# Kernel tuning notes

Measured on AMD Instinct MI355X. Metric: run time of the kernel, lower is better.

The kernel has to match this reference:

```python
import jax, jax.numpy as jnp
import numpy as np

N_NODES = 100000
N_EDGES = 3200000


def gcn_conv(x, src, dst, W, b, n):
    # x: [N, Fin] -> linear transform then symmetric-normalized scatter-add (PyG GCNConv)
    xw = x @ W  # [N, Fout]
    loop = jnp.arange(n, dtype=src.dtype)
    s = jnp.concatenate([src, loop])  # add self-loops
    d = jnp.concatenate([dst, loop])
    deg = jax.ops.segment_sum(jnp.ones_like(s, dtype=xw.dtype), d, num_segments=n)
    dinv = jnp.where(deg > 0, jax.lax.rsqrt(deg), 0.0)
    norm = dinv[s] * dinv[d]  # [E+N]
    out = jax.ops.segment_sum(xw[s] * norm[:, None], d, num_segments=n)
    return out + b


def setup_inputs() -> dict:
    key = jax.random.key(0)
    ks = jax.random.split(key, 11)
    x = jax.random.normal(ks[0], (N_NODES, 2), dtype=jnp.float32)
    edge_index = jax.random.randint(ks[1], (2, N_EDGES), 0, N_NODES, dtype=jnp.int64)
    W1 = jax.random.normal(ks[2], (2, 32), dtype=jnp.float32) * 0.5
    b1 = jax.random.normal(ks[3], (32,), dtype=jnp.float32) * 0.1
    W2 = jax.random.normal(ks[4], (32, 32), dtype=jnp.float32) * 0.18
    b2 = jax.random.normal(ks[5], (32,), dtype=jnp.float32) * 0.1
    Wf1 = jax.random.normal(ks[6], (32, 32), dtype=jnp.float32) * 0.18
    bf1 = jax.random.normal(ks[7], (32,), dtype=jnp.float32) * 0.1
    Wf2 = jax.random.normal(ks[8], (32, 1), dtype=jnp.float32) * 0.18
    bf2 = jax.random.normal(ks[9], (1,), dtype=jnp.float32) * 0.1
    return {"x": x, "edge_index": edge_index, "W1": W1, "b1": b1, "W2": W2,
            "b2": b2, "Wf1": Wf1, "bf1": bf1, "Wf2": Wf2, "bf2": bf2}


def reference(x, edge_index, W1, b1, W2, b2, Wf1, bf1, Wf2, bf2):
    n = x.shape[0]
    src, dst = edge_index[0], edge_index[1]
    h = jax.nn.relu(gcn_conv(x, src, dst, W1, b1, n))
    h = jax.nn.relu(gcn_conv(h, src, dst, W2, b2, n))
    h = jax.nn.relu(h @ Wf1 + bf1)
    return h @ Wf2 + bf2  # [N, 1]
```

## Files before the change

### kernel.cpp

```cpp
#include <hip/hip_runtime.h>

#define NGRP 512
#define CAP  6656
#define EPB  8192
#define NE   16
#define SRC_BITS 17
#define SRC_MASK 0x1FFFF

static __device__ __forceinline__ unsigned short f2bf(float f) {
    unsigned u = __float_as_uint(f);
    return (unsigned short)((u + 0x7FFFu + ((u >> 16) & 1u)) >> 16);
}
static __device__ __forceinline__ float bf2f_lo(unsigned u) { return __uint_as_float(u << 16); }
static __device__ __forceinline__ float bf2f_hi(unsigned u) { return __uint_as_float(u & 0xFFFF0000u); }


__global__ void k_init(int* gcursor) {
    gcursor[threadIdx.x] = threadIdx.x * CAP;
}

__global__ __launch_bounds__(512) void k_partition(const int* __restrict__ ei, int* gcursor,
                                                   unsigned* __restrict__ pairs,
                                                   int E, int n, int GN) {
    __shared__ int cnt[NGRP];
    __shared__ int cur[NGRP];
    int tid = threadIdx.x;
    cnt[tid] = 0;
    __syncthreads();
    int base = blockIdx.x * EPB;
    int sreg[NE], dreg[NE];
#pragma unroll
    for (int k = 0; k < NE; ++k) {
        int e = base + tid + k * 512;
        int d = -1, s = 0;
        if (e < E) {
            s = ei[e];
            d = ei[E + e];
            if ((unsigned)s < (unsigned)n && (unsigned)d < (unsigned)n)
                atomicAdd(&cnt[d / GN], 1);
            else d = -1;
        }
        sreg[k] = s; dreg[k] = d;
    }
    __syncthreads();
    { int c = cnt[tid]; cur[tid] = c ? atomicAdd(&gcursor[tid], c) : 0; }
    __syncthreads();
#pragma unroll
    for (int k = 0; k < NE; ++k) {
        int d = dreg[k];
        if (d >= 0) {
            int g = d / GN;
            int w = atomicAdd(&cur[g], 1);
            if (w < (g + 1) * CAP)
                pairs[w] = ((unsigned)(d - g * GN) << SRC_BITS) | (unsigned)sreg[k];
        }
    }
}

__global__ __launch_bounds__(512) void k_build(const int* __restrict__ gcursor,
                                               const unsigned* __restrict__ pairs,
                                               const float2* __restrict__ x2,
                                               int* __restrict__ rowStart, int* __restrict__ rowEnd,
                                               int* __restrict__ srclist, float* __restrict__ dinv,
                                               float2* __restrict__ z, int n, int GN) {
    __shared__ unsigned pl[CAP];
    __shared__ int cnt[512];
    __shared__ int cur[512];
    int g = blockIdx.x;
    int t = threadIdx.x;
    int gbeg = g * CAP;
    int gend = gcursor[g];
    int cape = gbeg + CAP;
    if (gend > cape) gend = cape;
    int m = gend - gbeg;
    cnt[t] = 0;
    __syncthreads();
    for (int k = t; k < m; k += 512) {
        unsigned v = pairs[gbeg + k];
        pl[k] = v;
        atomicAdd(&cnt[(v >> SRC_BITS) & 511], 1);
    }
    __syncthreads();
    int c = cnt[t];
    for (int off = 1; off < 512; off <<= 1) {
        int add = (t >= off) ? cnt[t - off] : 0;
        __syncthreads();
        cnt[t] += add;
        __syncthreads();
    }
    int excl = cnt[t] - c;
    int node = g * GN + t;
    if (t < GN && node < n) {
        int st = gbeg + excl;
        rowStart[node] = st;
        rowEnd[node] = st + c;
        float di = rsqrtf(1.0f + (float)c);
        dinv[node] = di;
        float2 xv = x2[node];
        z[node] = make_float2(xv.x * di, xv.y * di);
    }
    cur[t] = excl;
    __syncthreads();
    for (int k = t; k < m; k += 512) {
        unsigned v = pl[k];
        int dl = (v >> SRC_BITS) & 511;
        int pos = atomicAdd(&cur[dl], 1);
        srclist[gbeg + pos] = (int)(v & SRC_MASK);
    }
}


__global__ __launch_bounds__(256) void k_gather2f(const int* __restrict__ rowStart,
                                                  const int* __restrict__ rowEnd,
                                                  const int* __restrict__ srclist,
                                                  const float2* __restrict__ z,
                                                  float2* __restrict__ agg, int n) {
    int w = blockIdx.x * 256 + threadIdx.x;
    if (w >= n) return;
    int e = rowStart[w], end = rowEnd[w];
    float ax = 0.f, ay = 0.f;
    for (; e + 4 <= end; e += 4) {
        int s0 = srclist[e], s1 = srclist[e + 1], s2 = srclist[e + 2], s3 = srclist[e + 3];
        float2 v0 = z[s0], v1 = z[s1], v2 = z[s2], v3 = z[s3];
        ax += v0.x + v1.x + v2.x + v3.x;
        ay += v0.y + v1.y + v2.y + v3.y;
    }
    for (; e < end; ++e) {
        float2 v = z[srclist[e]];
        ax += v.x; ay += v.y;
    }
    float2 v = z[w];
    agg[w] = make_float2(ax + v.x, ay + v.y);
}

__global__ void k_mid1(const float2* __restrict__ agg, const float* __restrict__ dinv,
                       const float* __restrict__ W1, const float* __restrict__ b1,
                       const float* __restrict__ W2, unsigned short* __restrict__ y0,
                       unsigned short* __restrict__ y1, int n) {
    __shared__ float sW[1024];
    __shared__ float sh[8][33];
    int tid = threadIdx.x;
    for (int k = tid; k < 1024; k += 256) sW[k] = W2[k];
    int ln = tid >> 5, f = tid & 31;
    int i = blockIdx.x * 8 + ln;
    float h = 0.f, di = 0.f;
    if (i < n) {
        di = dinv[i];
        float2 a = agg[i];
        h = di * (a.x * W1[f] + a.y * W1[32 + f]) + b1[f];
        h = h > 0.f ? h : 0.f;
    }
    sh[ln][f] = h;
    __syncthreads();
    if (i < n) {
        float acc = 0.f;
#pragma unroll
        for (int k = 0; k < 32; ++k) acc += sh[ln][k] * sW[k * 32 + f];
        unsigned short* yp = (f < 16) ? y0 : y1;
        yp[(size_t)i * 16 + (f & 15)] = f2bf(acc * di);
    }
}

#define ACC8(v)                                        \
    a0 += bf2f_lo((v).x); a1 += bf2f_hi((v).x);        \
    a2 += bf2f_lo((v).y); a3 += bf2f_hi((v).y);        \
    a4 += bf2f_lo((v).z); a5 += bf2f_hi((v).z);        \
    a6 += bf2f_lo((v).w); a7 += bf2f_hi((v).w);

__global__ __launch_bounds__(256) void k_gather_plane(const int* __restrict__ rowStart,
                                                      const int* __restrict__ rowEnd,
                                                      const int* __restrict__ srclist,
                                                      const uint4* __restrict__ yh,
                                                      float4* __restrict__ acc4, int n, int p) {
    int w = blockIdx.x * 64 + (threadIdx.x >> 2);
    if (w >= n) return;
    int slot = (threadIdx.x >> 1) & 1;
    int q = threadIdx.x & 1;
    int beg = rowStart[w], end = rowEnd[w];
    int deg = end - beg;
    int half = (deg + 1) >> 1;
    int e = beg + slot * half;
    int e1 = slot ? end : (beg + half);
    float a0 = 0.f, a1 = 0.f, a2 = 0.f, a3 = 0.f, a4 = 0.f, a5 = 0.f, a6 = 0.f, a7 = 0.f;
    for (; e + 4 <= e1; e += 4) {
        int s0 = srclist[e], s1 = srclist[e + 1], s2 = srclist[e + 2], s3 = srclist[e + 3];
        uint4 v0 = yh[(size_t)s0 * 2 + q];
        uint4 v1 = yh[(size_t)s1 * 2 + q];
        uint4 v2 = yh[(size_t)s2 * 2 + q];
        uint4 v3 = yh[(size_t)s3 * 2 + q];
        ACC8(v0); ACC8(v1); ACC8(v2); ACC8(v3);
    }
    for (; e < e1; ++e) {
        uint4 v = yh[(size_t)srclist[e] * 2 + q];
        ACC8(v);
    }
    if (slot == 0) {
        uint4 v = yh[(size_t)w * 2 + q];
        ACC8(v);
    }
    a0 += __shfl_xor(a0, 2, 64);
    a1 += __shfl_xor(a1, 2, 64);
    a2 += __shfl_xor(a2, 2, 64);
    a3 += __shfl_xor(a3, 2, 64);
    a4 += __shfl_xor(a4, 2, 64);
    a5 += __shfl_xor(a5, 2, 64);
    a6 += __shfl_xor(a6, 2, 64);
    a7 += __shfl_xor(a7, 2, 64);
    if (slot == 0) {
        float4* dst = acc4 + (size_t)w * 8 + p * 4 + q * 2;
        dst[0] = make_float4(a0, a1, a2, a3);
        dst[1] = make_float4(a4, a5, a6, a7);
    }
}

__global__ void k_final(const float* __restrict__ acc, const float* __restrict__ dinv,
                        const float* __restrict__ b2, const float* __restrict__ Wf1,
                        const float* __restrict__ bf1, const float* __restrict__ Wf2,
                        const float* __restrict__ bf2, float* __restrict__ out, int n) {
    __shared__ float sW[1024];
    __shared__ float sh[8][33];
    int tid = threadIdx.x;
    for (int k = tid; k < 1024; k += 256) sW[k] = Wf1[k];
    int ln = tid >> 5, f = tid & 31;
    int i = blockIdx.x * 8 + ln;
    float h = 0.f;
    if (i < n) {
        h = dinv[i] * acc[(size_t)i * 32 + f] + b2[f];
        h = h > 0.f ? h : 0.f;
    }
    sh[ln][f] = h;
    __syncthreads();
    float p = 0.f;
    if (i < n) {
        float a = bf1[f];
#pragma unroll
        for (int k = 0; k < 32; ++k) a += sh[ln][k] * sW[k * 32 + f];
        a = a > 0.f ? a : 0.f;
        p = a * Wf2[f];
    }
#pragma unroll
    for (int m = 16; m >= 1; m >>= 1) p += __shfl_xor(p, m, 64);
    if (f == 0 && i < n) out[i] = p + bf2[0];
}


extern "C" void kernel_launch(void* const* d_in, const int* in_sizes, int n_in,
                              void* d_out, int out_size, void* d_ws, size_t ws_size,
                              hipStream_t stream) {
    const float* x   = (const float*)d_in[0];
    const int*   ei  = (const int*)d_in[1];
    const float* W1  = (const float*)d_in[2];
    const float* b1  = (const float*)d_in[3];
    const float* W2  = (const float*)d_in[4];
    const float* b2  = (const float*)d_in[5];
    const float* Wf1 = (const float*)d_in[6];
    const float* bf1 = (const float*)d_in[7];
    const float* Wf2 = (const float*)d_in[8];
    const float* bf2 = (const float*)d_in[9];
    float* out = (float*)d_out;

    int n = in_sizes[0] / 2;
    int E = in_sizes[1] / 2;
    int GN = (n + NGRP - 1) / NGRP;

    float* wsf = (float*)d_ws;
    int*    srclist  = (int*)wsf;
    size_t  o = (size_t)NGRP * CAP;
    int*    rowStart = (int*)(wsf + o);     o += n;
    int*    rowEnd   = (int*)(wsf + o);     o += n;
    float*  dinv     = wsf + o;             o += n;
    float2* z        = (float2*)(wsf + o);  o += 2 * (size_t)n;
    float2* agg      = (float2*)(wsf + o);  o += 2 * (size_t)n;
    int*    gcursor  = (int*)(wsf + o);     o += NGRP;
    o = (o + 3) & ~(size_t)3;
    float*  acc      = wsf + o;             o += 32 * (size_t)n;
    unsigned short* y0 = (unsigned short*)(wsf + o);
    unsigned short* y1 = y0 + (size_t)n * 16;
    unsigned* pairs = (unsigned*)acc;

    const int B = 256;
    int nblk = (E + EPB - 1) / EPB;

    k_init<<<1, NGRP, 0, stream>>>(gcursor);
    k_partition<<<nblk, 512, 0, stream>>>(ei, gcursor, pairs, E, n, GN);
    k_build<<<NGRP, 512, 0, stream>>>(gcursor, pairs, (const float2*)x, rowStart, rowEnd,
                                      srclist, dinv, z, n, GN);

    k_gather2f<<<(n + 255) / 256, B, 0, stream>>>(rowStart, rowEnd, srclist, z, agg, n);
    k_mid1<<<(n + 7) / 8, B, 0, stream>>>(agg, dinv, W1, b1, W2, y0, y1, n);

    k_gather_plane<<<(n + 63) / 64, B, 0, stream>>>(rowStart, rowEnd, srclist,
                                                    (const uint4*)y0, (float4*)acc, n, 0);
    k_gather_plane<<<(n + 63) / 64, B, 0, stream>>>(rowStart, rowEnd, srclist,
                                                    (const uint4*)y1, (float4*)acc, n, 1);

    k_final<<<(n + 7) / 8, B, 0, stream>>>(acc, dinv, b2, Wf1, bf1, Wf2, bf2, out, n);
}
```

Before: 174.5 us.

## Fuse layer-1 gather into mid kernel and merge both plane gathers into one launch

```diff
diff --git a/kernel.cpp b/kernel.cpp
--- a/kernel.cpp
+++ b/kernel.cpp
@@ -110,44 +110,41 @@
 }
 
 
-__global__ __launch_bounds__(256) void k_gather2f(const int* __restrict__ rowStart,
-                                                  const int* __restrict__ rowEnd,
-                                                  const int* __restrict__ srclist,
-                                                  const float2* __restrict__ z,
-                                                  float2* __restrict__ agg, int n) {
-    int w = blockIdx.x * 256 + threadIdx.x;
-    if (w >= n) return;
-    int e = rowStart[w], end = rowEnd[w];
-    float ax = 0.f, ay = 0.f;
-    for (; e + 4 <= end; e += 4) {
-        int s0 = srclist[e], s1 = srclist[e + 1], s2 = srclist[e + 2], s3 = srclist[e + 3];
-        float2 v0 = z[s0], v1 = z[s1], v2 = z[s2], v3 = z[s3];
-        ax += v0.x + v1.x + v2.x + v3.x;
-        ay += v0.y + v1.y + v2.y + v3.y;
-    }
-    for (; e < end; ++e) {
-        float2 v = z[srclist[e]];
-        ax += v.x; ay += v.y;
-    }
-    float2 v = z[w];
-    agg[w] = make_float2(ax + v.x, ay + v.y);
-}
-
-__global__ void k_mid1(const float2* __restrict__ agg, const float* __restrict__ dinv,
-                       const float* __restrict__ W1, const float* __restrict__ b1,
-                       const float* __restrict__ W2, unsigned short* __restrict__ y0,
-                       unsigned short* __restrict__ y1, int n) {
+__global__ __launch_bounds__(256) void k_mid1f(const int* __restrict__ rowStart,
+                                               const int* __restrict__ rowEnd,
+                                               const int* __restrict__ srclist,
+                                               const float2* __restrict__ z,
+                                               const float* __restrict__ dinv,
+                                               const float* __restrict__ W1,
+                                               const float* __restrict__ b1,
+                                               const float* __restrict__ W2,
+                                               unsigned short* __restrict__ y0,
+                                               unsigned short* __restrict__ y1, int n) {
     __shared__ float sW[1024];
     __shared__ float sh[8][33];
     int tid = threadIdx.x;
     for (int k = tid; k < 1024; k += 256) sW[k] = W2[k];
     int ln = tid >> 5, f = tid & 31;
     int i = blockIdx.x * 8 + ln;
+    float ax = 0.f, ay = 0.f;
+    if (i < n) {
+        int e = rowStart[i] + f, end = rowEnd[i];
+        for (; e < end; e += 32) {
+            float2 v = z[srclist[e]];
+            ax += v.x; ay += v.y;
+        }
+    }
+#pragma unroll
+    for (int m = 1; m < 32; m <<= 1) {
+        ax += __shfl_xor(ax, m, 64);
+        ay += __shfl_xor(ay, m, 64);
+    }
     float h = 0.f, di = 0.f;
     if (i < n) {
         di = dinv[i];
-        float2 a = agg[i];
-        h = di * (a.x * W1[f] + a.y * W1[32 + f]) + b1[f];
+        float2 zz = z[i];
+        ax += zz.x; ay += zz.y;
+        h = di * (ax * W1[f] + ay * W1[32 + f]) + b1[f];
         h = h > 0.f ? h : 0.f;
     }
     sh[ln][f] = h;
@@ -156,8 +153,8 @@
         float acc = 0.f;
 #pragma unroll
         for (int k = 0; k < 32; ++k) acc += sh[ln][k] * sW[k * 32 + f];
-        unsigned short* yp = (f < 16) ? y0 : y1;
-        yp[(size_t)i * 16 + (f & 15)] = f2bf(acc * di);
+        unsigned short* ypl = (f < 16) ? y0 : y1;
+        ypl[(size_t)i * 16 + (f & 15)] = f2bf(acc * di);
     }
 }
 
@@ -167,12 +164,16 @@
     a4 += bf2f_lo((v).z); a5 += bf2f_hi((v).z);        \
     a6 += bf2f_lo((v).w); a7 += bf2f_hi((v).w);
 
-__global__ __launch_bounds__(256) void k_gather_plane(const int* __restrict__ rowStart,
-                                                      const int* __restrict__ rowEnd,
-                                                      const int* __restrict__ srclist,
-                                                      const uint4* __restrict__ yh,
-                                                      float4* __restrict__ acc4, int n, int p) {
-    int w = blockIdx.x * 64 + (threadIdx.x >> 2);
+__global__ __launch_bounds__(256) void k_gather_planes(const int* __restrict__ rowStart,
+                                                       const int* __restrict__ rowEnd,
+                                                       const int* __restrict__ srclist,
+                                                       const uint4* __restrict__ yp0,
+                                                       const uint4* __restrict__ yp1,
+                                                       float4* __restrict__ acc4, int n, int nb) {
+    int p = (blockIdx.x >= nb) ? 1 : 0;
+    int b = blockIdx.x - p * nb;
+    const uint4* yh = p ? yp1 : yp0;
+    int w = b * 64 + (threadIdx.x >> 2);
     if (w >= n) return;
     int slot = (threadIdx.x >> 1) & 1;
     int q = threadIdx.x & 1;
@@ -270,7 +271,6 @@
     int*    rowEnd   = (int*)(wsf + o);     o += n;
     float*  dinv     = wsf + o;             o += n;
     float2* z        = (float2*)(wsf + o);  o += 2 * (size_t)n;
-    float2* agg      = (float2*)(wsf + o);  o += 2 * (size_t)n;
     int*    gcursor  = (int*)(wsf + o);     o += NGRP;
     o = (o + 3) & ~(size_t)3;
     float*  acc      = wsf + o;             o += 32 * (size_t)n;
@@ -278,21 +278,20 @@
     unsigned short* y1 = y0 + (size_t)n * 16;
     unsigned* pairs = (unsigned*)acc;
 
-    const int B = 256;
     int nblk = (E + EPB - 1) / EPB;
+    int nb = (n + 63) / 64;
 
     k_init<<<1, NGRP, 0, stream>>>(gcursor);
     k_partition<<<nblk, 512, 0, stream>>>(ei, gcursor, pairs, E, n, GN);
     k_build<<<NGRP, 512, 0, stream>>>(gcursor, pairs, (const float2*)x, rowStart, rowEnd,
                                       srclist, dinv, z, n, GN);
 
-    k_gather2f<<<(n + 255) / 256, B, 0, stream>>>(rowStart, rowEnd, srclist, z, agg, n);
-    k_mid1<<<(n + 7) / 8, B, 0, stream>>>(agg, dinv, W1, b1, W2, y0, y1, n);
-
-    k_gather_plane<<<(n + 63) / 64, B, 0, stream>>>(rowStart, rowEnd, srclist,
-                                                    (const uint4*)y0, (float4*)acc, n, 0);
-    k_gather_plane<<<(n + 63) / 64, B, 0, stream>>>(rowStart, rowEnd, srclist,
-                                                    (const uint4*)y1, (float4*)acc, n, 1);
-
-    k_final<<<(n + 7) / 8, B, 0, stream>>>(acc, dinv, b2, Wf1, bf1, Wf2, bf2, out, n);
-}
+    k_mid1f<<<(n + 7) / 8, 256, 0, stream>>>(rowStart, rowEnd, srclist, z, dinv,
+                                             W1, b1, W2, y0, y1, n);
+
+    k_gather_planes<<<2 * nb, 256, 0, stream>>>(rowStart, rowEnd, srclist,
+                                                (const uint4*)y0, (const uint4*)y1,
+                                                (float4*)acc, n, nb);
+
+    k_final<<<(n + 7) / 8, 256, 0, stream>>>(acc, dinv, b2, Wf1, bf1, Wf2, bf2, out, n);
+}
```

Measured after the change: 164.0 us. 1.06x faster.
